# Optimization experiments

Measured on AMD Instinct MI355X. Metric: run time of the kernel, lower is better.

The kernel has to match this reference:

```python
import jax, jax.numpy as jnp
import numpy as np

N_HEADS = 8
LN_EPS = 1e-5


def _layernorm(x, g, b):
    mu = jnp.mean(x, axis=-1, keepdims=True)
    var = jnp.var(x, axis=-1, keepdims=True)
    return (x - mu) * jax.lax.rsqrt(var + LN_EPS) * g + b


def _mha(xq, xkv, W, bvec):
    # W: [4, D, D] stacked (Wq, Wk, Wv, Wo); bvec: [4, D]
    Wq, Wk, Wv, Wo = W[0], W[1], W[2], W[3]
    bq, bk, bv, bo = bvec[0], bvec[1], bvec[2], bvec[3]
    B, Lq, D = xq.shape
    Lk = xkv.shape[1]
    dh = D // N_HEADS
    q = (xq @ Wq + bq).reshape(B, Lq, N_HEADS, dh)
    k = (xkv @ Wk + bk).reshape(B, Lk, N_HEADS, dh)
    v = (xkv @ Wv + bv).reshape(B, Lk, N_HEADS, dh)
    scores = jnp.einsum('bqhd,bkhd->bhqk', q, k) / jnp.sqrt(jnp.asarray(dh, xq.dtype))
    attn = jax.nn.softmax(scores, axis=-1)
    out = jnp.einsum('bhqk,bkhd->bqhd', attn, v).reshape(B, Lq, D)
    return out @ Wo + bo


def setup_inputs() -> dict:
    key = jax.random.key(0)
    ks = jax.random.split(key, 8)
    B, A, D, F = 64, 512, 256, 512
    s = 0.02
    return {
        'trg': jax.random.normal(ks[0], (B, A, D), jnp.float32),
        'src': jax.random.normal(ks[1], (B, A, D), jnp.float32),
        'W_sa': jax.random.normal(ks[2], (4, D, D), jnp.float32) * s,
        'b_sa': jnp.zeros((4, D), jnp.float32),
        'W_ea': jax.random.normal(ks[3], (4, D, D), jnp.float32) * s,
        'b_ea': jnp.zeros((4, D), jnp.float32),
        'ln_g': jnp.ones((D,), jnp.float32),
        'ln_b': jnp.zeros((D,), jnp.float32),
        'W_fc1': jax.random.normal(ks[4], (D, F), jnp.float32) * s,
        'b_fc1': jnp.zeros((F,), jnp.float32),
        'W_fc2': jax.random.normal(ks[5], (F, F), jnp.float32) * s,
        'b_fc2': jnp.zeros((F,), jnp.float32),
        'W_out': jax.random.normal(ks[6], (F, 2), jnp.float32) * s,
        'b_out': jnp.zeros((2,), jnp.float32),
    }


def reference(trg, src, W_sa, b_sa, W_ea, b_ea, ln_g, ln_b,
              W_fc1, b_fc1, W_fc2, b_fc2, W_out, b_out):
    # n_layers = 1 decoder layer: self-attn + cross-attn, residual + LayerNorm
    h = _layernorm(trg + _mha(trg, trg, W_sa, b_sa), ln_g, ln_b)
    h = _layernorm(h + _mha(h, src, W_ea, b_ea), ln_g, ln_b)
    # norm+softmax weighted-sum pooling (fused replacement of the double loop)
    atom_norm = jnp.linalg.norm(h, axis=2)            # [B, A]
    w = jax.nn.softmax(atom_norm, axis=1)             # [B, A]
    pooled = jnp.einsum('ba,bad->bd', w, h)           # [B, D]
    # fc stack (dropout is identity in eval mode)
    h1 = jax.nn.relu(pooled @ W_fc1 + b_fc1)
    h2 = jax.nn.relu(h1 @ W_fc2 + b_fc2)
    return h2 @ W_out + b_out                          # [B, 2]
```

## Files before the change

kernel.cpp:

```cpp
#include <hip/hip_runtime.h>

typedef unsigned short u16;
typedef __attribute__((ext_vector_type(8))) short s16x8;
typedef __attribute__((ext_vector_type(8))) _Float16 f16x8;
typedef __attribute__((ext_vector_type(4))) float f32x4;

#define ASYNC16(gp, lp) \
  __builtin_amdgcn_global_load_lds((__attribute__((address_space(1))) void*)(gp), \
                                   (__attribute__((address_space(3))) void*)(lp), 16, 0, 0)

__device__ __forceinline__ u16 f2h(float f) {
  _Float16 h = (_Float16)f;
  union { _Float16 h; u16 u; } v; v.h = h;
  return v.u;
}
__device__ __forceinline__ float h2f(u16 s) {
  union { _Float16 h; u16 u; } v; v.u = s; return (float)v.h;
}

__device__ __forceinline__ int swz4(int row) { return (row & 3) ^ ((row >> 2) & 3); }

__global__ __launch_bounds__(256) void prep_kernel(
    const float* __restrict__ trg, const float* __restrict__ src,
    const float* __restrict__ Wsa, const float* __restrict__ Wea,
    u16* __restrict__ trg_h, u16* __restrict__ src_h, u16* __restrict__ wt)
{
  int blk = blockIdx.x, tid = threadIdx.x;
  if (blk < 8192) {
    const float* sp = (blk < 4096) ? trg : src;
    u16* dp = (blk < 4096) ? trg_h : src_h;
    size_t base = ((size_t)(blk & 4095) * 256 + tid) * 8;
    float4 a = *(const float4*)(sp + base);
    float4 c = *(const float4*)(sp + base + 4);
    s16x8 o;
    o[0] = (short)f2h(a.x); o[1] = (short)f2h(a.y);
    o[2] = (short)f2h(a.z); o[3] = (short)f2h(a.w);
    o[4] = (short)f2h(c.x); o[5] = (short)f2h(c.y);
    o[6] = (short)f2h(c.z); o[7] = (short)f2h(c.w);
    *(s16x8*)(dp + base) = o;
  } else {
    int t = (blk - 8192) * 256 + tid;
    int row = t >> 8, k = t & 255;
    const float* W; int sel, col;
    if (row < 768)       { W = Wsa; sel = row >> 8;              col = row & 255; }
    else if (row < 1024) { W = Wsa; sel = 3;                     col = row & 255; }
    else if (row < 1280) { W = Wea; sel = 0;                     col = row & 255; }
    else if (row < 1792) { W = Wea; sel = ((row - 1280) >> 8) + 1; col = (row - 1280) & 255; }
    else                 { W = Wea; sel = 3;                     col = row & 255; }
    wt[(size_t)row * 256 + k] = f2h(W[sel * 65536 + k * 256 + col]);
  }
}

__global__ __launch_bounds__(256, 3) void gemm_bias_f16(
    const u16* __restrict__ A, const u16* __restrict__ Bt,
    const float* __restrict__ bias, u16* __restrict__ C, int N)
{
  __shared__ u16 Asm[128 * 32];
  __shared__ u16 Bsm[128 * 32];
  const int tid = threadIdx.x;
  const int wv = tid >> 6, ln = tid & 63;
  const int quad = ln >> 4, l16 = ln & 15;
  const int nblk = blockIdx.x;
  const size_t arow0 = (size_t)blockIdx.y * 128;
  const size_t brow0 = (size_t)nblk * 128;
  const int wr = wv >> 1, wc = wv & 1;
  f32x4 acc[4][4];
  const f32x4 VZERO = {0.f, 0.f, 0.f, 0.f};
#pragma unroll
  for (int i = 0; i < 4; ++i)
#pragma unroll
    for (int j = 0; j < 4; ++j) acc[i][j] = VZERO;

  for (int k0 = 0; k0 < 256; k0 += 32) {
    __syncthreads();
#pragma unroll
    for (int j = 0; j < 2; ++j) {
      int c = (j * 4 + wv) * 64 + ln;
      int row = c >> 2, slot = c & 3;
      int kc = slot ^ swz4(row);
      ASYNC16(A + (arow0 + row) * 256 + k0 + kc * 8, Asm + c * 8);
      ASYNC16(Bt + (brow0 + row) * 256 + k0 + kc * 8, Bsm + c * 8);
    }
    __syncthreads();
    f16x8 af[4], bfr[4];
#pragma unroll
    for (int mt = 0; mt < 4; ++mt) {
      int tr = wr * 64 + mt * 16 + l16;
      int slot = quad ^ swz4(tr);
      af[mt] = *(const f16x8*)(Asm + (tr * 4 + slot) * 8);
    }
#pragma unroll
    for (int nt = 0; nt < 4; ++nt) {
      int tr = wc * 64 + nt * 16 + l16;
      int slot = quad ^ swz4(tr);
      bfr[nt] = *(const f16x8*)(Bsm + (tr * 4 + slot) * 8);
    }
#pragma unroll
    for (int mt = 0; mt < 4; ++mt)
#pragma unroll
      for (int nt = 0; nt < 4; ++nt)
        acc[mt][nt] = __builtin_amdgcn_mfma_f32_16x16x32_f16(af[mt], bfr[nt], acc[mt][nt], 0, 0, 0);
  }
#pragma unroll
  for (int nt = 0; nt < 4; ++nt) {
    int col = nblk * 128 + wc * 64 + nt * 16 + l16;
    float bz = bias[col];
#pragma unroll
    for (int mt = 0; mt < 4; ++mt) {
      size_t row0 = arow0 + wr * 64 + mt * 16 + quad * 4;
#pragma unroll
      for (int r = 0; r < 4; ++r)
        C[(row0 + r) * (size_t)N + col] = f2h(acc[mt][nt][r] + bz);
    }
  }
}

__global__ __launch_bounds__(256, 3) void attn_mfma(
    const u16* __restrict__ Qp, int ldq,
    const u16* __restrict__ Kp, int ldk,
    const u16* __restrict__ Vp, int ldv,
    u16* __restrict__ Op)
{
  __shared__ u16 Ks[256 * 40];
  __shared__ u16 Vt[32 * 264];
  __shared__ __align__(16) unsigned Pw[4][32 * 20];
  const int tid = threadIdx.x;
  const int wv = tid >> 6, ln = tid & 63;
  const int quad = ln >> 4, l16 = ln & 15;
  const int lin = blockIdx.x;
  const int qb = (lin >> 3) & 3;
  const int g = ((lin >> 5) << 3) | (lin & 7);
  const int h = g & 7;
  const size_t rb = (size_t)(g >> 3) * 512;
  const f32x4 VZERO = {0.f, 0.f, 0.f, 0.f};

  f16x8 qf[2];
  const _Float16 qs = (_Float16)0.25503492f;
#pragma unroll
  for (int mq = 0; mq < 2; ++mq) {
    int qrow = qb * 128 + wv * 32 + mq * 16 + l16;
    qf[mq] = *(const f16x8*)(Qp + (rb + qrow) * (size_t)ldq + h * 32 + quad * 8);
#pragma unroll
    for (int j = 0; j < 8; ++j) qf[mq][j] *= qs;
  }
  f16x8 onesf;
#pragma unroll
  for (int j = 0; j < 8; ++j) onesf[j] = (_Float16)1.0f;

  f32x4 o[2][2], osum[2];
#pragma unroll
  for (int mq = 0; mq < 2; ++mq) { o[mq][0] = VZERO; o[mq][1] = VZERO; osum[mq] = VZERO; }

  for (int kb = 0; kb < 2; ++kb) {
    __syncthreads();
    for (int c = tid; c < 1024; c += 256) {
      int row = c >> 2, part = c & 3;
      s16x8 kv = *(const s16x8*)(Kp + (rb + kb * 256 + row) * (size_t)ldk + h * 32 + part * 8);
      *(s16x8*)(Ks + row * 40 + part * 8) = kv;
      s16x8 vv = *(const s16x8*)(Vp + (rb + kb * 256 + row) * (size_t)ldv + h * 32 + part * 8);
      int kts = row >> 5, l = row & 31;
      int p = 2 * (l & 15) + (l >> 4);
#pragma unroll
      for (int j = 0; j < 8; ++j) Vt[(part * 8 + j) * 264 + kts * 32 + p] = (u16)vv[j];
    }
    __syncthreads();
    for (int kt = 0; kt < 8; ++kt) {
      f16x8 kf0 = *(const f16x8*)(Ks + (kt * 32 + l16) * 40 + quad * 8);
      f16x8 kf1 = *(const f16x8*)(Ks + (kt * 32 + 16 + l16) * 40 + quad * 8);
      f16x8 vf0 = *(const f16x8*)(Vt + l16 * 264 + kt * 32 + quad * 8);
      f16x8 vf1 = *(const f16x8*)(Vt + (16 + l16) * 264 + kt * 32 + quad * 8);
#pragma unroll
      for (int mq = 0; mq < 2; ++mq) {
        f32x4 s0 = __builtin_amdgcn_mfma_f32_16x16x32_f16(qf[mq], kf0, VZERO, 0, 0, 0);
        f32x4 s1 = __builtin_amdgcn_mfma_f32_16x16x32_f16(qf[mq], kf1, VZERO, 0, 0, 0);
#pragma unroll
        for (int r = 0; r < 4; ++r) {
          float e0 = __builtin_amdgcn_exp2f(s0[r]);
          float e1 = __builtin_amdgcn_exp2f(s1[r]);
          union { _Float16 h2[2]; unsigned u; } pk;
          pk.h2[0] = (_Float16)e0; pk.h2[1] = (_Float16)e1;
          Pw[wv][(mq * 16 + quad * 4 + r) * 20 + l16] = pk.u;
        }
      }
#pragma unroll
      for (int mq = 0; mq < 2; ++mq) {
        f16x8 pf = *(const f16x8*)(&Pw[wv][(mq * 16 + l16) * 20 + quad * 4]);
        o[mq][0] = __builtin_amdgcn_mfma_f32_16x16x32_f16(pf, vf0, o[mq][0], 0, 0, 0);
        o[mq][1] = __builtin_amdgcn_mfma_f32_16x16x32_f16(pf, vf1, o[mq][1], 0, 0, 0);
        osum[mq] = __builtin_amdgcn_mfma_f32_16x16x32_f16(pf, onesf, osum[mq], 0, 0, 0);
      }
    }
  }
#pragma unroll
  for (int mq = 0; mq < 2; ++mq)
#pragma unroll
    for (int r = 0; r < 4; ++r) {
      float inv = 1.f / osum[mq][r];
      size_t row = rb + qb * 128 + wv * 32 + mq * 16 + quad * 4 + r;
      Op[row * 256 + h * 32 + l16]      = f2h(o[mq][0][r] * inv);
      Op[row * 256 + h * 32 + 16 + l16] = f2h(o[mq][1][r] * inv);
    }
}

__global__ __launch_bounds__(256, 3) void lnproj_kernel(
    const u16* __restrict__ A, const u16* __restrict__ Wt,
    const float* __restrict__ bo, const u16* __restrict__ resid,
    const float* __restrict__ g, const float* __restrict__ lb,
    u16* __restrict__ Hh, float* __restrict__ norms)
{
  __shared__ u16 Asm[64 * 32];
  __shared__ u16 Bsm[256 * 32];
  const int tid = threadIdx.x;
  const int wv = tid >> 6, ln = tid & 63;
  const int quad = ln >> 4, l16 = ln & 15;
  const size_t arow0 = (size_t)blockIdx.x * 64;
  f32x4 acc[16];
  const f32x4 VZERO = {0.f, 0.f, 0.f, 0.f};
#pragma unroll
  for (int nt = 0; nt < 16; ++nt) acc[nt] = VZERO;

  for (int k0 = 0; k0 < 256; k0 += 32) {
    __syncthreads();
    {
      int c = tid;
      int row = c >> 2, slot = c & 3;
      int kc = slot ^ swz4(row);
      ASYNC16(A + (arow0 + row) * 256 + k0 + kc * 8, Asm + c * 8);
    }
#pragma unroll
    for (int j = 0; j < 4; ++j) {
      int c = (j * 4 + wv) * 64 + ln;
      int row = c >> 2, slot = c & 3;
      int kc = slot ^ swz4(row);
      ASYNC16(Wt + (size_t)row * 256 + k0 + kc * 8, Bsm + c * 8);
    }
    __syncthreads();
    int tr = wv * 16 + l16;
    int aslot = quad ^ swz4(tr);
    f16x8 af = *(const f16x8*)(Asm + (tr * 4 + aslot) * 8);
#pragma unroll
    for (int nt = 0; nt < 16; ++nt) {
      int br = nt * 16 + l16;
      int bslot = quad ^ swz4(br);
      f16x8 bfr = *(const f16x8*)(Bsm + (br * 4 + bslot) * 8);
      acc[nt] = __builtin_amdgcn_mfma_f32_16x16x32_f16(af, bfr, acc[nt], 0, 0, 0);
    }
  }
  float gv[16], bv[16], bov[16];
#pragma unroll
  for (int nt = 0; nt < 16; ++nt) {
    int col = nt * 16 + l16;
    gv[nt] = g[col]; bv[nt] = lb[col]; bov[nt] = bo[col];
  }
#pragma unroll
  for (int r = 0; r < 4; ++r) {
    size_t row = arow0 + wv * 16 + quad * 4 + r;
    const u16* rrow = resid + row * 256;
    float vals[16]; float s = 0.f;
#pragma unroll
    for (int nt = 0; nt < 16; ++nt) {
      float v = acc[nt][r] + bov[nt] + h2f(rrow[nt * 16 + l16]);
      vals[nt] = v; s += v;
    }
#pragma unroll
    for (int m = 1; m < 16; m <<= 1) s += __shfl_xor(s, m);
    float mean = s * (1.f / 256.f);
    float sq = 0.f;
#pragma unroll
    for (int nt = 0; nt < 16; ++nt) { float d = vals[nt] - mean; sq = fmaf(d, d, sq); }
#pragma unroll
    for (int m = 1; m < 16; m <<= 1) sq += __shfl_xor(sq, m);
    float rstd = rsqrtf(sq * (1.f / 256.f) + 1e-5f);
    float ssq = 0.f;
#pragma unroll
    for (int nt = 0; nt < 16; ++nt) {
      float hv = (vals[nt] - mean) * rstd * gv[nt] + bv[nt];
      Hh[row * 256 + nt * 16 + l16] = f2h(hv);
      ssq = fmaf(hv, hv, ssq);
    }
    if (norms) {
#pragma unroll
      for (int m = 1; m < 16; m <<= 1) ssq += __shfl_xor(ssq, m);
      if (l16 == 0) norms[row] = sqrtf(ssq);
    }
  }
}

__global__ __launch_bounds__(256) void softmax_kernel(const float* norms, float* w,
                                                      float* __restrict__ pooled)
{
  int b = blockIdx.x, tid = threadIdx.x;
  int ln = tid & 63, wvi = tid >> 6;
  __shared__ float red[8];
  const float* nb = norms + b * 512;
  float n0 = nb[tid], n1 = nb[tid + 256];
  float mx = fmaxf(n0, n1);
#pragma unroll
  for (int m = 1; m < 64; m <<= 1) mx = fmaxf(mx, __shfl_xor(mx, m));
  if (ln == 0) red[wvi] = mx;
  __syncthreads();
  mx = fmaxf(fmaxf(red[0], red[1]), fmaxf(red[2], red[3]));
  float e0 = __expf(n0 - mx), e1 = __expf(n1 - mx);
  float s = e0 + e1;
#pragma unroll
  for (int m = 1; m < 64; m <<= 1) s += __shfl_xor(s, m);
  if (ln == 0) red[4 + wvi] = s;
  __syncthreads();
  s = red[4] + red[5] + red[6] + red[7];
  float inv = 1.f / s;
  w[b * 512 + tid] = e0 * inv;
  w[b * 512 + tid + 256] = e1 * inv;
  pooled[b * 256 + tid] = 0.f;
}

__global__ __launch_bounds__(256) void poolsum_kernel(const float* __restrict__ w,
                                                      const u16* __restrict__ h,
                                                      float* __restrict__ pooled)
{
  int b = blockIdx.x, sl = blockIdx.y, d = threadIdx.x;
  const u16* hb = h + ((size_t)b * 512 + sl * 64) * 256 + d;
  const float* wb = w + b * 512 + sl * 64;
  float acc = 0.f;
#pragma unroll 8
  for (int a = 0; a < 64; ++a) acc = fmaf(wb[a], h2f(hb[(size_t)a * 256]), acc);
  atomicAdd(&pooled[b * 256 + d], acc);
}

__global__ __launch_bounds__(512) void fc1_kernel(
    const float* __restrict__ pooled, const float* __restrict__ Wfc1,
    const float* __restrict__ bfc1, float* __restrict__ x1)
{
  int b = blockIdx.x, tid = threadIdx.x;
  __shared__ float px[256];
  if (tid < 256) px[tid] = pooled[b * 256 + tid];
  __syncthreads();
  float a = bfc1[tid];
#pragma unroll 8
  for (int d = 0; d < 256; ++d) a = fmaf(px[d], Wfc1[d * 512 + tid], a);
  x1[b * 512 + tid] = fmaxf(a, 0.f);
}

__global__ __launch_bounds__(512) void fc23_kernel(
    const float* __restrict__ x1, const float* __restrict__ Wfc2,
    const float* __restrict__ bfc2, const float* __restrict__ Wout,
    const float* __restrict__ bout, float* __restrict__ out)
{
  int b = blockIdx.x, tid = threadIdx.x;
  __shared__ float sx[512];
  __shared__ float rr[16];
  sx[tid] = x1[b * 512 + tid];
  __syncthreads();
  float a = bfc2[tid];
#pragma unroll 8
  for (int d = 0; d < 512; ++d) a = fmaf(sx[d], Wfc2[d * 512 + tid], a);
  a = fmaxf(a, 0.f);
  float p0 = a * Wout[tid * 2];
  float p1 = a * Wout[tid * 2 + 1];
  int ln = tid & 63, wvi = tid >> 6;
#pragma unroll
  for (int m = 1; m < 64; m <<= 1) { p0 += __shfl_xor(p0, m); p1 += __shfl_xor(p1, m); }
  if (ln == 0) { rr[wvi] = p0; rr[8 + wvi] = p1; }
  __syncthreads();
  if (tid == 0) {
    float s = 0.f;
#pragma unroll
    for (int i = 0; i < 8; ++i) s += rr[i];
    out[b * 2] = s + bout[0];
  }
  if (tid == 1) {
    float s = 0.f;
#pragma unroll
    for (int i = 0; i < 8; ++i) s += rr[8 + i];
    out[b * 2 + 1] = s + bout[1];
  }
}

extern "C" void kernel_launch(void* const* d_in, const int* in_sizes, int n_in,
                              void* d_out, int out_size, void* d_ws, size_t ws_size,
                              hipStream_t stream) {
  const float* trg  = (const float*)d_in[0];
  const float* src  = (const float*)d_in[1];
  const float* Wsa  = (const float*)d_in[2];
  const float* bsa  = (const float*)d_in[3];
  const float* Wea  = (const float*)d_in[4];
  const float* bea  = (const float*)d_in[5];
  const float* lng  = (const float*)d_in[6];
  const float* lnb  = (const float*)d_in[7];
  const float* Wfc1 = (const float*)d_in[8];
  const float* bfc1 = (const float*)d_in[9];
  const float* Wfc2 = (const float*)d_in[10];
  const float* bfc2 = (const float*)d_in[11];
  const float* Wout = (const float*)d_in[12];
  const float* bout = (const float*)d_in[13];
  float* out = (float*)d_out;

  const size_t M = 32768;
  char* ws = (char*)d_ws;
  u16* trg_h = (u16*)ws;                ws += M * 256 * 2;
  u16* src_h = (u16*)ws;                ws += M * 256 * 2;
  u16* wt     = (u16*)ws;               ws += 2048 * 256 * 2;
  u16* qkv    = (u16*)ws;               ws += M * 768 * 2;
  u16* attnb  = (u16*)ws;               ws += M * 256 * 2;
  u16* hh     = (u16*)ws;               ws += M * 256 * 2;
  u16* h2h    = (u16*)ws;               ws += M * 256 * 2;
  float* norms = (float*)ws;            ws += M * 4;
  float* pooled = (float*)ws;           ws += 64 * 256 * 4;
  float* x1buf = (float*)ws;            ws += 64 * 512 * 4;

  u16* wt_sa_qkv = wt;
  u16* wt_sa_o   = wt + 768 * 256;
  u16* wt_ea_q   = wt + 1024 * 256;
  u16* wt_ea_kv  = wt + 1280 * 256;
  u16* wt_ea_o   = wt + 1792 * 256;
  u16* kvb = qkv + M * 256;

  prep_kernel<<<10240, 256, 0, stream>>>(trg, src, Wsa, Wea, trg_h, src_h, wt);
  gemm_bias_f16<<<dim3(6, 256), 256, 0, stream>>>(trg_h, wt_sa_qkv, bsa, qkv, 768);
  attn_mfma<<<2048, 256, 0, stream>>>(qkv, 768, qkv + 256, 768, qkv + 512, 768, attnb);
  lnproj_kernel<<<512, 256, 0, stream>>>(attnb, wt_sa_o, bsa + 768, trg_h, lng, lnb,
                                         hh, nullptr);
  gemm_bias_f16<<<dim3(2, 256), 256, 0, stream>>>(hh, wt_ea_q, bea, qkv, 256);
  gemm_bias_f16<<<dim3(4, 256), 256, 0, stream>>>(src_h, wt_ea_kv, bea + 256, kvb, 512);
  attn_mfma<<<2048, 256, 0, stream>>>(qkv, 256, kvb, 512, kvb + 256, 512, attnb);
  lnproj_kernel<<<512, 256, 0, stream>>>(attnb, wt_ea_o, bea + 768, hh, lng, lnb,
                                         h2h, norms);
  softmax_kernel<<<64, 256, 0, stream>>>(norms, norms, pooled);
  poolsum_kernel<<<dim3(64, 8), 256, 0, stream>>>(norms, h2h, pooled);
  fc1_kernel<<<64, 512, 0, stream>>>(pooled, Wfc1, bfc1, x1buf);
  fc23_kernel<<<64, 512, 0, stream>>>(x1buf, Wfc2, bfc2, Wout, bout, out);

  (void)in_sizes; (void)n_in; (void)out_size; (void)ws_size;
}
```

Baseline: 350.3 us.

## Keep attention probabilities in registers via transposed S and permlane swaps

Computes the score tile as K·Q^T so the exp'd probabilities land in a layout that, after v_permlane32/16 swaps, matches the A-operand layout for the P·V MFMA. This removes the per-wave LDS staging buffer for P (its stores, loads and the wave-level ordering between them) and simplifies the V transpose store layout accordingly. Freeing that LDS also lets the launch bound request 4 blocks per SM instead of 3, at the cost of tighter register limits and some cross-lane permute instructions.

```diff
diff --git a/kernel.cpp b/kernel.cpp
--- a/kernel.cpp
+++ b/kernel.cpp
@@ -115,7 +115,7 @@
   }
 }
 
-__global__ __launch_bounds__(256, 3) void attn_mfma(
+__global__ __launch_bounds__(256, 4) void attn_mfma(
     const u16* __restrict__ Qp, int ldq,
     const u16* __restrict__ Kp, int ldk,
     const u16* __restrict__ Vp, int ldv,
@@ -123,7 +123,6 @@
 {
   __shared__ u16 Ks[256 * 40];
   __shared__ u16 Vt[32 * 264];
-  __shared__ __align__(16) unsigned Pw[4][32 * 20];
   const int tid = threadIdx.x;
   const int wv = tid >> 6, ln = tid & 63;
   const int quad = ln >> 4, l16 = ln & 15;
@@ -159,9 +158,8 @@
       *(s16x8*)(Ks + row * 40 + part * 8) = kv;
       s16x8 vv = *(const s16x8*)(Vp + (rb + kb * 256 + row) * (size_t)ldv + h * 32 + part * 8);
       int kts = row >> 5, l = row & 31;
-      int p = 2 * (l & 15) + (l >> 4);
-#pragma unroll
-      for (int j = 0; j < 8; ++j) Vt[(part * 8 + j) * 264 + kts * 32 + p] = (u16)vv[j];
+#pragma unroll
+      for (int j = 0; j < 8; ++j) Vt[(part * 8 + j) * 264 + kts * 32 + l] = (u16)vv[j];
     }
     __syncthreads();
     for (int kt = 0; kt < 8; ++kt) {
@@ -171,20 +169,25 @@
       f16x8 vf1 = *(const f16x8*)(Vt + (16 + l16) * 264 + kt * 32 + quad * 8);
 #pragma unroll
       for (int mq = 0; mq < 2; ++mq) {
-        f32x4 s0 = __builtin_amdgcn_mfma_f32_16x16x32_f16(qf[mq], kf0, VZERO, 0, 0, 0);
-        f32x4 s1 = __builtin_amdgcn_mfma_f32_16x16x32_f16(qf[mq], kf1, VZERO, 0, 0, 0);
-#pragma unroll
-        for (int r = 0; r < 4; ++r) {
-          float e0 = __builtin_amdgcn_exp2f(s0[r]);
-          float e1 = __builtin_amdgcn_exp2f(s1[r]);
-          union { _Float16 h2[2]; unsigned u; } pk;
-          pk.h2[0] = (_Float16)e0; pk.h2[1] = (_Float16)e1;
-          Pw[wv][(mq * 16 + quad * 4 + r) * 20 + l16] = pk.u;
-        }
-      }
-#pragma unroll
-      for (int mq = 0; mq < 2; ++mq) {
-        f16x8 pf = *(const f16x8*)(&Pw[wv][(mq * 16 + l16) * 20 + quad * 4]);
+        f32x4 s0 = __builtin_amdgcn_mfma_f32_16x16x32_f16(kf0, qf[mq], VZERO, 0, 0, 0);
+        f32x4 s1 = __builtin_amdgcn_mfma_f32_16x16x32_f16(kf1, qf[mq], VZERO, 0, 0, 0);
+        union { _Float16 h2[2]; unsigned u; } pk0, pk1, pk2, pk3;
+        pk0.h2[0] = (_Float16)__builtin_amdgcn_exp2f(s0[0]);
+        pk0.h2[1] = (_Float16)__builtin_amdgcn_exp2f(s0[1]);
+        pk1.h2[0] = (_Float16)__builtin_amdgcn_exp2f(s0[2]);
+        pk1.h2[1] = (_Float16)__builtin_amdgcn_exp2f(s0[3]);
+        pk2.h2[0] = (_Float16)__builtin_amdgcn_exp2f(s1[0]);
+        pk2.h2[1] = (_Float16)__builtin_amdgcn_exp2f(s1[1]);
+        pk3.h2[0] = (_Float16)__builtin_amdgcn_exp2f(s1[2]);
+        pk3.h2[1] = (_Float16)__builtin_amdgcn_exp2f(s1[3]);
+        unsigned c0 = pk0.u, c1 = pk1.u, c2 = pk2.u, c3 = pk3.u;
+        asm("v_permlane32_swap_b32 %0, %1" : "+v"(c0), "+v"(c2));
+        asm("v_permlane32_swap_b32 %0, %1" : "+v"(c1), "+v"(c3));
+        asm("v_permlane16_swap_b32 %0, %1" : "+v"(c0), "+v"(c2));
+        asm("v_permlane16_swap_b32 %0, %1" : "+v"(c1), "+v"(c3));
+        union { unsigned u[4]; f16x8 f; } P;
+        P.u[0] = c0; P.u[1] = c1; P.u[2] = c2; P.u[3] = c3;
+        f16x8 pf = P.f;
         o[mq][0] = __builtin_amdgcn_mfma_f32_16x16x32_f16(pf, vf0, o[mq][0], 0, 0, 0);
         o[mq][1] = __builtin_amdgcn_mfma_f32_16x16x32_f16(pf, vf1, o[mq][1], 0, 0, 0);
         osum[mq] = __builtin_amdgcn_mfma_f32_16x16x32_f16(pf, onesf, osum[mq], 0, 0, 0);
```

New measurement: 346.3 us. About the same (-1.1%).

## Keep attention probabilities in registers via permlane swaps and transpose-read V from LDS

Applied to the files above, without the earlier changes.

The attention kernel now computes S transposed (K as the A operand), packs exp2 results with cvt_pkrtz, and rearranges them into the PV operand layout with v_permlane32/16 swaps. This removes the per-wave LDS round trip for P. V is stored row-major with plain 16-byte stores and read with ds_read_b64_tr_b16, replacing the scalar transposed scatter. The smaller LDS footprint allows raising the occupancy hint from 3 to 4 blocks. In exchange it relies on gfx950-specific instructions, an explicit waitcnt and a sched_barrier, and pkrtz rounds toward zero instead of to nearest.

```diff
diff --git a/kernel.cpp b/kernel.cpp
--- a/kernel.cpp
+++ b/kernel.cpp
@@ -3,11 +3,17 @@
 typedef unsigned short u16;
 typedef __attribute__((ext_vector_type(8))) short s16x8;
 typedef __attribute__((ext_vector_type(8))) _Float16 f16x8;
+typedef __attribute__((ext_vector_type(4))) _Float16 f16x4;
+typedef __attribute__((ext_vector_type(2))) __fp16 fp16x2;
 typedef __attribute__((ext_vector_type(4))) float f32x4;
 
 #define ASYNC16(gp, lp) \
   __builtin_amdgcn_global_load_lds((__attribute__((address_space(1))) void*)(gp), \
                                    (__attribute__((address_space(3))) void*)(lp), 16, 0, 0)
+
+#define TR16(dst, p, OFF) \
+  asm volatile("ds_read_b64_tr_b16 %0, %1 offset:" #OFF \
+               : "=v"(dst) : "v"((__attribute__((address_space(3))) const u16*)(p)))
 
 __device__ __forceinline__ u16 f2h(float f) {
   _Float16 h = (_Float16)f;
@@ -19,6 +25,12 @@
 }
 
 __device__ __forceinline__ int swz4(int row) { return (row & 3) ^ ((row >> 2) & 3); }
+
+__device__ __forceinline__ unsigned pkrtz_u32(float lo, float hi) {
+  union { fp16x2 h; unsigned u; } v;
+  v.h = __builtin_amdgcn_cvt_pkrtz(lo, hi);
+  return v.u;
+}
 
 __global__ __launch_bounds__(256) void prep_kernel(
     const float* __restrict__ trg, const float* __restrict__ src,
@@ -115,15 +127,14 @@
   }
 }
 
-__global__ __launch_bounds__(256, 3) void attn_mfma(
+__global__ __launch_bounds__(256, 4) void attn_mfma(
     const u16* __restrict__ Qp, int ldq,
     const u16* __restrict__ Kp, int ldk,
     const u16* __restrict__ Vp, int ldv,
     u16* __restrict__ Op)
 {
   __shared__ u16 Ks[256 * 40];
-  __shared__ u16 Vt[32 * 264];
-  __shared__ __align__(16) unsigned Pw[4][32 * 20];
+  __shared__ u16 Vs[8192];
   const int tid = threadIdx.x;
   const int wv = tid >> 6, ln = tid & 63;
   const int quad = ln >> 4, l16 = ln & 15;
@@ -158,36 +169,48 @@
       s16x8 kv = *(const s16x8*)(Kp + (rb + kb * 256 + row) * (size_t)ldk + h * 32 + part * 8);
       *(s16x8*)(Ks + row * 40 + part * 8) = kv;
       s16x8 vv = *(const s16x8*)(Vp + (rb + kb * 256 + row) * (size_t)ldv + h * 32 + part * 8);
-      int kts = row >> 5, l = row & 31;
-      int p = 2 * (l & 15) + (l >> 4);
-#pragma unroll
-      for (int j = 0; j < 8; ++j) Vt[(part * 8 + j) * 264 + kts * 32 + p] = (u16)vv[j];
+      *(s16x8*)(Vs + (row >> 2) * 128 + (part >> 1) * 64 + (row & 3) * 16 + (part & 1) * 8) = vv;
     }
     __syncthreads();
     for (int kt = 0; kt < 8; ++kt) {
       f16x8 kf0 = *(const f16x8*)(Ks + (kt * 32 + l16) * 40 + quad * 8);
       f16x8 kf1 = *(const f16x8*)(Ks + (kt * 32 + 16 + l16) * 40 + quad * 8);
-      f16x8 vf0 = *(const f16x8*)(Vt + l16 * 264 + kt * 32 + quad * 8);
-      f16x8 vf1 = *(const f16x8*)(Vt + (16 + l16) * 264 + kt * 32 + quad * 8);
+      const u16* vb = Vs + (kt * 8 + quad * 2) * 128 + l16 * 4;
+      f16x4 v00, v01, v10, v11;
+      TR16(v00, vb, 0);
+      TR16(v01, vb, 256);
+      TR16(v10, vb, 128);
+      TR16(v11, vb, 384);
+      f16x8 pf[2];
 #pragma unroll
       for (int mq = 0; mq < 2; ++mq) {
-        f32x4 s0 = __builtin_amdgcn_mfma_f32_16x16x32_f16(qf[mq], kf0, VZERO, 0, 0, 0);
-        f32x4 s1 = __builtin_amdgcn_mfma_f32_16x16x32_f16(qf[mq], kf1, VZERO, 0, 0, 0);
-#pragma unroll
-        for (int r = 0; r < 4; ++r) {
-          float e0 = __builtin_amdgcn_exp2f(s0[r]);
-          float e1 = __builtin_amdgcn_exp2f(s1[r]);
-          union { _Float16 h2[2]; unsigned u; } pk;
-          pk.h2[0] = (_Float16)e0; pk.h2[1] = (_Float16)e1;
-          Pw[wv][(mq * 16 + quad * 4 + r) * 20 + l16] = pk.u;
-        }
+        f32x4 s0 = __builtin_amdgcn_mfma_f32_16x16x32_f16(kf0, qf[mq], VZERO, 0, 0, 0);
+        f32x4 s1 = __builtin_amdgcn_mfma_f32_16x16x32_f16(kf1, qf[mq], VZERO, 0, 0, 0);
+        unsigned u0 = pkrtz_u32(__builtin_amdgcn_exp2f(s0[0]),
+                                __builtin_amdgcn_exp2f(s0[1]));
+        unsigned u1 = pkrtz_u32(__builtin_amdgcn_exp2f(s0[2]),
+                                __builtin_amdgcn_exp2f(s0[3]));
+        unsigned u2 = pkrtz_u32(__builtin_amdgcn_exp2f(s1[0]),
+                                __builtin_amdgcn_exp2f(s1[1]));
+        unsigned u3 = pkrtz_u32(__builtin_amdgcn_exp2f(s1[2]),
+                                __builtin_amdgcn_exp2f(s1[3]));
+        asm("v_permlane32_swap_b32 %0, %1" : "+v"(u0), "+v"(u2));
+        asm("v_permlane32_swap_b32 %0, %1" : "+v"(u1), "+v"(u3));
+        asm("v_permlane16_swap_b32 %0, %1" : "+v"(u0), "+v"(u2));
+        asm("v_permlane16_swap_b32 %0, %1" : "+v"(u1), "+v"(u3));
+        union { unsigned u[4]; f16x8 f; } P;
+        P.u[0] = u0; P.u[1] = u1; P.u[2] = u2; P.u[3] = u3;
+        pf[mq] = P.f;
       }
+      asm volatile("s_waitcnt lgkmcnt(0)" ::: "memory");
+      __builtin_amdgcn_sched_barrier(0);
+      f16x8 vf0 = __builtin_shufflevector(v00, v01, 0, 1, 2, 3, 4, 5, 6, 7);
+      f16x8 vf1 = __builtin_shufflevector(v10, v11, 0, 1, 2, 3, 4, 5, 6, 7);
 #pragma unroll
       for (int mq = 0; mq < 2; ++mq) {
-        f16x8 pf = *(const f16x8*)(&Pw[wv][(mq * 16 + l16) * 20 + quad * 4]);
-        o[mq][0] = __builtin_amdgcn_mfma_f32_16x16x32_f16(pf, vf0, o[mq][0], 0, 0, 0);
-        o[mq][1] = __builtin_amdgcn_mfma_f32_16x16x32_f16(pf, vf1, o[mq][1], 0, 0, 0);
-        osum[mq] = __builtin_amdgcn_mfma_f32_16x16x32_f16(pf, onesf, osum[mq], 0, 0, 0);
+        o[mq][0] = __builtin_amdgcn_mfma_f32_16x16x32_f16(pf[mq], vf0, o[mq][0], 0, 0, 0);
+        o[mq][1] = __builtin_amdgcn_mfma_f32_16x16x32_f16(pf[mq], vf1, o[mq][1], 0, 0, 0);
+        osum[mq] = __builtin_amdgcn_mfma_f32_16x16x32_f16(pf[mq], onesf, osum[mq], 0, 0, 0);
       }
     }
   }
```

Result: faster. 328.9 us (-6.1%).
